# Performance work log

Hardware: AMD Instinct MI355X
Metric: run time of the kernel (lower is better)

The kernel has to match this reference:

```python
import jax, jax.numpy as jnp
import numpy as np

FEATS_DIM = 64
N_CELLS = 50000
N_GENES = 20000
N_EDGES = 3000000


def setup_inputs() -> dict:
    key = jax.random.key(0)
    ks = jax.random.split(key, 12)
    c_feat = jax.random.normal(ks[0], (N_CELLS, FEATS_DIM), dtype=jnp.float32)
    g_feat = jax.random.normal(ks[1], (N_GENES, FEATS_DIM), dtype=jnp.float32)
    cs_factor = jax.random.uniform(ks[2], (N_CELLS, 1), dtype=jnp.float32)
    gs_factor = jax.random.uniform(ks[3], (N_GENES, 1), dtype=jnp.float32)
    edge_u = jax.random.randint(ks[4], (N_EDGES,), 0, N_CELLS, dtype=jnp.int32)
    edge_v = jax.random.randint(ks[5], (N_EDGES,), 0, N_GENES, dtype=jnp.int32)
    s = 1.0 / np.sqrt(FEATS_DIM)
    W_mean = jax.random.uniform(ks[6], (FEATS_DIM, 1), jnp.float32, -s, s)
    b_mean = jax.random.uniform(ks[7], (1,), jnp.float32, -s, s)
    W_disp = jax.random.uniform(ks[8], (FEATS_DIM, 1), jnp.float32, -s, s)
    b_disp = jax.random.uniform(ks[9], (1,), jnp.float32, -s, s)
    W_pi = jax.random.uniform(ks[10], (FEATS_DIM, 1), jnp.float32, -s, s)
    b_pi = jax.random.uniform(ks[11], (1,), jnp.float32, -s, s)
    return {
        "c_feat": c_feat, "g_feat": g_feat,
        "cs_factor": cs_factor, "gs_factor": gs_factor,
        "edge_u": edge_u, "edge_v": edge_v,
        "W_mean": W_mean, "b_mean": b_mean,
        "W_disp": W_disp, "b_disp": b_disp,
        "W_pi": W_pi, "b_pi": b_pi,
    }


def reference(c_feat, g_feat, cs_factor, gs_factor, edge_u, edge_v,
              W_mean, b_mean, W_disp, b_disp, W_pi, b_pi):
    # edge gather: h_d[e] = c_feat[src(e)] * g_feat[dst(e)]  -> [E, d]
    h_d = c_feat[edge_u] * g_feat[edge_v]
    # per-edge factors gathered from node data -> [E, 1]
    gs_e = gs_factor[edge_v]
    cs_e = cs_factor[edge_u]
    # tiny d->1 linears
    mu_ = jax.nn.sigmoid(h_d @ W_mean + b_mean)      # dec_mean
    disp_ = h_d @ W_disp + b_disp                     # dec_disp
    pi = jax.nn.sigmoid(h_d @ W_pi + b_pi)            # dec_pi
    # DispAct: clamp(softplus(x), 1e-4, 1e4)
    disp = jnp.clip(jax.nn.softplus(gs_e * disp_), 1e-4, 1e4)
    # MeanAct: clamp(exp(x)-1, 1e-5, 1e6)
    mu = cs_e * jnp.clip(jnp.exp(gs_e * mu_) - 1.0, 1e-5, 1e6)
    return (mu, disp, pi)
```

## Files before the change

### kernel.cpp

```cpp
#include <hip/hip_runtime.h>
#include <math.h>


typedef _Float16 h2 __attribute__((ext_vector_type(2)));

#if __has_builtin(__builtin_amdgcn_fdot2)
__device__ __forceinline__ float fdot2f(h2 a, h2 b, float c) {
    return __builtin_amdgcn_fdot2(a, b, c, false);
}
#else
__device__ __forceinline__ float fdot2f(h2 a, h2 b, float c) {
    return fmaf((float)a.x, (float)b.x, fmaf((float)a.y, (float)b.y, c));
}
#endif

__device__ __forceinline__ float red8(float x) {
    int t;
    t = __builtin_amdgcn_mov_dpp(__float_as_int(x), 0xB1, 0xF, 0xF, true);
    x += __int_as_float(t);
    t = __builtin_amdgcn_mov_dpp(__float_as_int(x), 0x4E, 0xF, 0xF, true);
    x += __int_as_float(t);
    t = __builtin_amdgcn_mov_dpp(__float_as_int(x), 0x141, 0xF, 0xF, true);
    x += __int_as_float(t);
    return x;
}

__device__ __forceinline__ unsigned pack2h(float lo, float hi) {
    h2 p = {(_Float16)lo, (_Float16)hi};
    return __builtin_bit_cast(unsigned, p);
}

__global__ __launch_bounds__(256) void zinb_pack_kernel(
    const float4* __restrict__ c_src, const float4* __restrict__ g_src,
    uint4* __restrict__ c_dst, uint4* __restrict__ g_dst,
    int n_c_groups, int n_total_groups)
{
    const int i = (int)(blockIdx.x * blockDim.x + threadIdx.x);
    if (i >= n_total_groups) return;
    const float4* src; uint4* dst; int j;
    if (i < n_c_groups) { src = c_src; dst = c_dst; j = i; }
    else                { src = g_src; dst = g_dst; j = i - n_c_groups; }
    const float4 a = src[2 * j];
    const float4 b = src[2 * j + 1];
    uint4 o;
    o.x = pack2h(a.x, a.y);
    o.y = pack2h(a.z, a.w);
    o.z = pack2h(b.x, b.y);
    o.w = pack2h(b.z, b.w);
    dst[j] = o;
}

__global__ __launch_bounds__(256, 8) void zinb_edge_f16_kernel(
    const uint4* __restrict__ c_pack,
    const uint4* __restrict__ g_pack,
    const float* __restrict__ cs_factor,
    const float* __restrict__ gs_factor,
    const int* __restrict__ edge_u,
    const int* __restrict__ edge_v,
    const float* __restrict__ W_mean, const float* __restrict__ b_mean,
    const float* __restrict__ W_disp, const float* __restrict__ b_disp,
    const float* __restrict__ W_pi,   const float* __restrict__ b_pi,
    float* __restrict__ out_mu,
    float* __restrict__ out_disp,
    float* __restrict__ out_pi,
    int n_edges)
{
    const int lane = (int)(threadIdx.x & 63);
    const int k    = lane & 7;
    const int grp  = lane >> 3;

    h2 wm[4], wd[4], wp[4];
    #pragma unroll
    for (int i = 0; i < 4; ++i) {
        wm[i] = (h2){(_Float16)W_mean[8 * k + 2 * i], (_Float16)W_mean[8 * k + 2 * i + 1]};
        wd[i] = (h2){(_Float16)W_disp[8 * k + 2 * i], (_Float16)W_disp[8 * k + 2 * i + 1]};
        wp[i] = (h2){(_Float16)W_pi  [8 * k + 2 * i], (_Float16)W_pi  [8 * k + 2 * i + 1]};
    }
    const float bm = b_mean[0], bd = b_disp[0], bp = b_pi[0];

    const int perm = (k << 3) | grp;

    int e0 = (int)(blockIdx.x * blockDim.x + threadIdx.x) & ~63;
    const int stride = (int)(gridDim.x * blockDim.x);

    for (; e0 < n_edges; e0 += stride) {
        const int et  = e0 + perm;
        const int etc = (et < n_edges) ? et : (n_edges - 1);
        const int ut = edge_u[etc];
        const int vt = edge_v[etc];
        const float cs_t = cs_factor[ut];
        const float gs_t = gs_factor[vt];

        int ej0 = e0 + grp;
        if (ej0 >= n_edges) ej0 = n_edges - 1;
        uint4 cu4 = c_pack[(size_t)edge_u[ej0] * 8 + k];
        uint4 gu4 = g_pack[(size_t)edge_v[ej0] * 8 + k];

        float pmk = 0.f, pdk = 0.f, ppk = 0.f;

        #pragma unroll
        for (int j = 0; j < 8; ++j) {
            uint4 ncu, ngu;
            if (j < 7) {
                int en = e0 + 8 * (j + 1) + grp;
                if (en >= n_edges) en = n_edges - 1;
                ncu = c_pack[(size_t)edge_u[en] * 8 + k];
                ngu = g_pack[(size_t)edge_v[en] * 8 + k];
            }

            const h2 c0 = __builtin_bit_cast(h2, cu4.x), g0 = __builtin_bit_cast(h2, gu4.x);
            const h2 c1 = __builtin_bit_cast(h2, cu4.y), g1 = __builtin_bit_cast(h2, gu4.y);
            const h2 c2 = __builtin_bit_cast(h2, cu4.z), g2 = __builtin_bit_cast(h2, gu4.z);
            const h2 c3 = __builtin_bit_cast(h2, cu4.w), g3 = __builtin_bit_cast(h2, gu4.w);
            const h2 h0 = c0 * g0;
            const h2 h1 = c1 * g1;
            const h2 hh2 = c2 * g2;
            const h2 h3 = c3 * g3;

            float pm = 0.f, pd = 0.f, pp = 0.f;
            pm = fdot2f(h0, wm[0], pm); pm = fdot2f(h1, wm[1], pm);
            pm = fdot2f(hh2, wm[2], pm); pm = fdot2f(h3, wm[3], pm);
            pd = fdot2f(h0, wd[0], pd); pd = fdot2f(h1, wd[1], pd);
            pd = fdot2f(hh2, wd[2], pd); pd = fdot2f(h3, wd[3], pd);
            pp = fdot2f(h0, wp[0], pp); pp = fdot2f(h1, wp[1], pp);
            pp = fdot2f(hh2, wp[2], pp); pp = fdot2f(h3, wp[3], pp);

            pm = red8(pm);
            pd = red8(pd);
            pp = red8(pp);

            if (k == j) { pmk = pm; pdk = pd; ppk = pp; }

            cu4 = ncu; gu4 = ngu;
        }

        const float mu_ = __builtin_amdgcn_rcpf(1.f + __expf(-(pmk + bm)));
        const float pi_ = __builtin_amdgcn_rcpf(1.f + __expf(-(ppk + bp)));

        const float sx = gs_t * (pdk + bd);
        const float sp = fmaxf(sx, 0.f) + __logf(1.f + __expf(-fabsf(sx)));
        const float disp = fminf(fmaxf(sp, 1e-4f), 1e4f);

        const float mu = cs_t * fminf(fmaxf(__expf(gs_t * mu_) - 1.f, 1e-5f), 1e6f);

        if (et < n_edges) {
            __builtin_nontemporal_store(mu,   out_mu + et);
            __builtin_nontemporal_store(disp, out_disp + et);
            __builtin_nontemporal_store(pi_,  out_pi + et);
        }
    }
}

__global__ __launch_bounds__(256) void zinb_edge_f32_kernel(
    const float* __restrict__ c_feat,
    const float* __restrict__ g_feat,
    const float* __restrict__ cs_factor,
    const float* __restrict__ gs_factor,
    const int* __restrict__ edge_u,
    const int* __restrict__ edge_v,
    const float* __restrict__ W_mean, const float* __restrict__ b_mean,
    const float* __restrict__ W_disp, const float* __restrict__ b_disp,
    const float* __restrict__ W_pi,   const float* __restrict__ b_pi,
    float* __restrict__ out_mu,
    float* __restrict__ out_disp,
    float* __restrict__ out_pi,
    int n_edges)
{
    __shared__ float4 wlds[48];
    {
        const int t = threadIdx.x;
        if (t < 48) {
            const int which = t / 16;
            const int kk    = t % 16;
            const float4* src = (which == 0) ? (const float4*)W_mean
                              : (which == 1) ? (const float4*)W_disp
                                             : (const float4*)W_pi;
            wlds[kk * 3 + which] = src[kk];
        }
    }
    __syncthreads();

    const float bm = b_mean[0], bd = b_disp[0], bp = b_pi[0];
    const float4* __restrict__ c4 = (const float4*)c_feat;
    const float4* __restrict__ g4 = (const float4*)g_feat;

    const int tid    = (int)(blockIdx.x * blockDim.x + threadIdx.x);
    const int stride = (int)(gridDim.x * blockDim.x);

    for (int e = tid; e < n_edges; e += stride) {
        const int u = edge_u[e];
        const int v = edge_v[e];
        const float4* __restrict__ cb = c4 + (size_t)u * 16;
        const float4* __restrict__ gb = g4 + (size_t)v * 16;

        float pm = 0.f, pd = 0.f, pp = 0.f;
        #pragma unroll
        for (int kk = 0; kk < 16; ++kk) {
            const float4 cc = cb[kk];
            const float4 gg = gb[kk];
            const float4 wmv = wlds[kk * 3 + 0];
            const float4 wdv = wlds[kk * 3 + 1];
            const float4 wpv = wlds[kk * 3 + 2];
            const float hx = cc.x * gg.x;
            const float hy = cc.y * gg.y;
            const float hz = cc.z * gg.z;
            const float hw = cc.w * gg.w;
            pm = fmaf(hx, wmv.x, fmaf(hy, wmv.y, fmaf(hz, wmv.z, fmaf(hw, wmv.w, pm))));
            pd = fmaf(hx, wdv.x, fmaf(hy, wdv.y, fmaf(hz, wdv.z, fmaf(hw, wdv.w, pd))));
            pp = fmaf(hx, wpv.x, fmaf(hy, wpv.y, fmaf(hz, wpv.z, fmaf(hw, wpv.w, pp))));
        }

        const float gs = gs_factor[v];
        const float cs = cs_factor[u];
        const float mu_ = __builtin_amdgcn_rcpf(1.f + __expf(-(pm + bm)));
        const float pi_ = __builtin_amdgcn_rcpf(1.f + __expf(-(pp + bp)));
        const float sx = gs * (pd + bd);
        const float sp = fmaxf(sx, 0.f) + __logf(1.f + __expf(-fabsf(sx)));
        const float disp = fminf(fmaxf(sp, 1e-4f), 1e4f);
        const float mu = cs * fminf(fmaxf(__expf(gs * mu_) - 1.f, 1e-5f), 1e6f);

        out_mu[e]   = mu;
        out_disp[e] = disp;
        out_pi[e]   = pi_;
    }
}

extern "C" void kernel_launch(void* const* d_in, const int* in_sizes, int n_in,
                              void* d_out, int out_size, void* d_ws, size_t ws_size,
                              hipStream_t stream) {
    const float* c_feat = (const float*)d_in[0];
    const float* g_feat = (const float*)d_in[1];
    const float* cs     = (const float*)d_in[2];
    const float* gs     = (const float*)d_in[3];
    const int*   eu     = (const int*)d_in[4];
    const int*   ev     = (const int*)d_in[5];
    const float* Wm     = (const float*)d_in[6];
    const float* bm     = (const float*)d_in[7];
    const float* Wd     = (const float*)d_in[8];
    const float* bd     = (const float*)d_in[9];
    const float* Wp     = (const float*)d_in[10];
    const float* bp     = (const float*)d_in[11];

    const int E       = in_sizes[4];
    const int n_cells = in_sizes[0] / 64;
    const int n_genes = in_sizes[1] / 64;

    float* out_mu   = (float*)d_out;
    float* out_disp = out_mu + E;
    float* out_pi   = out_mu + 2 * (size_t)E;

    const size_t c_bytes = (size_t)n_cells * 64 * 2;
    const size_t g_bytes = (size_t)n_genes * 64 * 2;

    if (ws_size >= c_bytes + g_bytes) {
        uint4* c_pack = (uint4*)d_ws;
        uint4* g_pack = (uint4*)((char*)d_ws + c_bytes);

        const int n_c_groups = n_cells * 8;
        const int n_total    = n_c_groups + n_genes * 8;
        dim3 pgrid((n_total + 255) / 256), pblock(256);
        hipLaunchKernelGGL(zinb_pack_kernel, pgrid, pblock, 0, stream,
                           (const float4*)c_feat, (const float4*)g_feat,
                           c_pack, g_pack, n_c_groups, n_total);

        dim3 grid(2048), block(256);
        hipLaunchKernelGGL(zinb_edge_f16_kernel, grid, block, 0, stream,
                           c_pack, g_pack, cs, gs, eu, ev,
                           Wm, bm, Wd, bd, Wp, bp,
                           out_mu, out_disp, out_pi, E);
    } else {
        dim3 grid(2048), block(256);
        hipLaunchKernelGGL(zinb_edge_f32_kernel, grid, block, 0, stream,
                           c_feat, g_feat, cs, gs, eu, ev,
                           Wm, bm, Wd, bd, Wp, bp,
                           out_mu, out_disp, out_pi, E);
    }
}
```

Baseline: 198.6 us.

## Issue all eight edge row gathers up front and drop occupancy bound

Replaces the one-ahead software prefetch of packed feature rows with a batch that first loads all eight edge indices, then issues all sixteen 16-byte row gathers before any compute. The aim is to raise memory-level parallelism on the random gathers, which are latency bound. It also removes the min-blocks hint of 8 from launch bounds, letting the compiler use more registers for the 16 uint4 buffers at the possible cost of fewer resident waves.

```diff
diff --git a/kernel.cpp b/kernel.cpp
--- a/kernel.cpp
+++ b/kernel.cpp
@@ -50,7 +50,7 @@
     dst[j] = o;
 }
 
-__global__ __launch_bounds__(256, 8) void zinb_edge_f16_kernel(
+__global__ __launch_bounds__(256) void zinb_edge_f16_kernel(
     const uint4* __restrict__ c_pack,
     const uint4* __restrict__ g_pack,
     const float* __restrict__ cs_factor,
@@ -84,34 +84,35 @@
     const int stride = (int)(gridDim.x * blockDim.x);
 
     for (; e0 < n_edges; e0 += stride) {
+        int ua[8], va[8];
+        #pragma unroll
+        for (int j = 0; j < 8; ++j) {
+            int ej = e0 + 8 * j + grp;
+            if (ej >= n_edges) ej = n_edges - 1;
+            ua[j] = edge_u[ej];
+            va[j] = edge_v[ej];
+        }
+
+        uint4 cu[8], gu[8];
+        #pragma unroll
+        for (int j = 0; j < 8; ++j) {
+            cu[j] = c_pack[(size_t)ua[j] * 8 + k];
+            gu[j] = g_pack[(size_t)va[j] * 8 + k];
+        }
+
         const int et  = e0 + perm;
         const int etc = (et < n_edges) ? et : (n_edges - 1);
-        const int ut = edge_u[etc];
-        const int vt = edge_v[etc];
-        const float cs_t = cs_factor[ut];
-        const float gs_t = gs_factor[vt];
-
-        int ej0 = e0 + grp;
-        if (ej0 >= n_edges) ej0 = n_edges - 1;
-        uint4 cu4 = c_pack[(size_t)edge_u[ej0] * 8 + k];
-        uint4 gu4 = g_pack[(size_t)edge_v[ej0] * 8 + k];
+        const float cs_t = cs_factor[edge_u[etc]];
+        const float gs_t = gs_factor[edge_v[etc]];
 
         float pmk = 0.f, pdk = 0.f, ppk = 0.f;
 
         #pragma unroll
         for (int j = 0; j < 8; ++j) {
-            uint4 ncu, ngu;
-            if (j < 7) {
-                int en = e0 + 8 * (j + 1) + grp;
-                if (en >= n_edges) en = n_edges - 1;
-                ncu = c_pack[(size_t)edge_u[en] * 8 + k];
-                ngu = g_pack[(size_t)edge_v[en] * 8 + k];
-            }
-
-            const h2 c0 = __builtin_bit_cast(h2, cu4.x), g0 = __builtin_bit_cast(h2, gu4.x);
-            const h2 c1 = __builtin_bit_cast(h2, cu4.y), g1 = __builtin_bit_cast(h2, gu4.y);
-            const h2 c2 = __builtin_bit_cast(h2, cu4.z), g2 = __builtin_bit_cast(h2, gu4.z);
-            const h2 c3 = __builtin_bit_cast(h2, cu4.w), g3 = __builtin_bit_cast(h2, gu4.w);
+            const h2 c0 = __builtin_bit_cast(h2, cu[j].x), g0 = __builtin_bit_cast(h2, gu[j].x);
+            const h2 c1 = __builtin_bit_cast(h2, cu[j].y), g1 = __builtin_bit_cast(h2, gu[j].y);
+            const h2 c2 = __builtin_bit_cast(h2, cu[j].z), g2 = __builtin_bit_cast(h2, gu[j].z);
+            const h2 c3 = __builtin_bit_cast(h2, cu[j].w), g3 = __builtin_bit_cast(h2, gu[j].w);
             const h2 h0 = c0 * g0;
             const h2 h1 = c1 * g1;
             const h2 hh2 = c2 * g2;
@@ -130,8 +131,6 @@
             pp = red8(pp);
 
             if (k == j) { pmk = pm; pdk = pd; ppk = pp; }
-
-            cu4 = ncu; gu4 = ngu;
         }
 
         const float mu_ = __builtin_amdgcn_rcpf(1.f + __expf(-(pmk + bm)));
```

Measured after the change: 184.7 us. 7.0% less time.
